# Performance work log

Hardware: AMD Instinct MI355X
Metric: run time of the kernel (lower is better)

Reference implementation:

```python
import jax, jax.numpy as jnp
import numpy as np
jax.config.update("jax_enable_x64", True)

B, S, E, H, L = 2, 1024, 768, 8, 8
FF, V = 2048, 32000
NT, REAL = 1, 512  # n_thoughts_taken, real_token_count


def _ln(x, g, b, eps=1e-5):
    m = jnp.mean(x, axis=-1, keepdims=True)
    v = jnp.var(x, axis=-1, keepdims=True)
    return (x - m) / jnp.sqrt(v + eps) * g + b


def setup_inputs() -> dict:
    key = jax.random.key(0)
    ks = jax.random.split(key, 12)
    f32 = jnp.float32
    rn = lambda k, shp, s=0.02: jax.random.normal(k, shp, f32) * s
    return {
        "x": jax.random.normal(ks[0], (B, S, E), f32),
        "tpe": rn(ks[1], (NT + 1, E)),
        "Wqkv": rn(ks[2], (L, 3 * E, E)),
        "bqkv": jnp.zeros((L, 3 * E), f32),
        "W1": rn(ks[3], (L, FF, E)),
        "b1": jnp.zeros((L, FF), f32),
        "W2": rn(ks[4], (L, E, FF)),
        "b2": jnp.zeros((L, E), f32),
        "g1": jnp.ones((L, E), f32),
        "be1": jnp.zeros((L, E), f32),
        "g2": jnp.ones((L, E), f32),
        "be2": jnp.zeros((L, E), f32),
        "gf": jnp.ones((E,), f32),
        "bf": jnp.zeros((E,), f32),
        "Wp1": rn(ks[5], (FF, E)),
        "bp1": jnp.zeros((FF,), f32),
        "Wp2": rn(ks[6], (V, FF)),
        "bp2": jnp.zeros((V,), f32),
        "Wv1": rn(ks[7], (FF, E)),
        "bv1": jnp.zeros((FF,), f32),
        "Wv2": rn(ks[8], (1, FF)),
        "bv2": jnp.zeros((1,), f32),
        "n_thoughts_taken": NT,
        "real_token_count": REAL,
    }


def reference(x, tpe, Wqkv, bqkv, W1, b1, W2, b2, g1, be1, g2, be2, gf, bf,
              Wp1, bp1, Wp2, bp2, Wv1, bv1, Wv2, bv2,
              n_thoughts_taken, real_token_count):
    Bs, Sq, Em = x.shape
    bs = int(n_thoughts_taken) + 1          # per-thought block size
    real = int(real_token_count)
    dh = Em // H

    # ---- DualPositionalEncoding (dropout=0) ----
    pos = np.arange(real)[:, None]
    div = np.exp(np.arange(0, Em, 2) * (-np.log(10000.0) / Em))
    pe = np.zeros((real, Em), np.float32)
    pe[:, 0::2] = np.sin(pos * div)
    pe[:, 1::2] = np.cos(pos * div)
    xb = x[:, :real * bs].reshape(Bs, real, bs, Em)
    xb = xb + jnp.asarray(pe)[None, :, None, :] + tpe[None, None, :bs, :]
    h = xb.reshape(Bs, real * bs, Em)
    pad = Sq - real * bs
    if pad > 0:
        h = jnp.pad(h, ((0, 0), (0, pad), (0, 0)))

    # ---- block-causal mask. NOTE: the original adds the BOOL mask to the
    # fp64 scores, so masked positions get +1.0 (not -inf). Faithful. ----
    i = np.arange(Sq)
    tok = i // bs
    p = i % bs
    M = ((tok[:, None] == tok[None, :]) & (p[None, :] >= p[:, None])) | \
        ((p[:, None] == 0) & (i[None, :] > i[:, None]) & (i[None, :] < real * bs))
    bias = jnp.asarray((M.T == 0).astype(np.float64))  # [S, S]
    scale = 1.0 / np.sqrt(dh)

    def layer(hc, params):
        Wq, bq, w1, b1_, w2, b2_, g1_, be1_, g2_, be2_ = params
        h64 = hc.astype(jnp.float64)
        qkv = h64 @ Wq.astype(jnp.float64).T + bq.astype(jnp.float64)
        q, k, v = jnp.split(qkv, 3, axis=-1)
        heads = lambda t: t.reshape(Bs, Sq, H, dh).transpose(0, 2, 1, 3)
        q, k, v = heads(q), heads(k), heads(v)
        scores = jnp.einsum('bhqd,bhkd->bhqk', q, k) * scale + bias
        w = jax.nn.softmax(scores, axis=-1)
        o = jnp.einsum('bhqk,bhkd->bhqd', w, v)
        o = o.transpose(0, 2, 1, 3).reshape(Bs, Sq, Em).astype(hc.dtype)
        # NOTE: original skips the attention out_proj entirely. Faithful.
        hc = _ln(hc + o, g1_, be1_)
        ff = jax.nn.gelu(hc @ w1.T + b1_, approximate=False) @ w2.T + b2_
        hc = _ln(hc + ff, g2_, be2_)
        return jnp.nan_to_num(hc), None

    h, _ = jax.lax.scan(layer, h, (Wqkv, bqkv, W1, b1, W2, b2, g1, be1, g2, be2))
    h = _ln(h, gf, bf)  # TransformerEncoder final norm

    act_idx = jnp.arange(real) * bs + n_thoughts_taken
    a = h[:, act_idx]  # [B, real, E]
    policy = jax.nn.gelu(a @ Wp1.T + bp1, approximate=False) @ Wp2.T + bp2
    value = jax.nn.gelu(a @ Wv1.T + bv1, approximate=False) @ Wv2.T + bv2
    return policy, value
```

## Files before the change

kernel.cpp:

```cpp
#include <hip/hip_runtime.h>
#include <math.h>

#define BB    2
#define SS    1024
#define EE    768
#define NH    8
#define DHD   96
#define NL    8
#define FFD   2048
#define VD    32000
#define REALC 512
#define MTOK  (BB*SS)
#define MACTN (BB*REALC)
#define QKVW  (3*EE)

#define QB 64
#define KB 64
#define KS_LD 104
#define VT_LD 72
#define P_LD  72

typedef __attribute__((ext_vector_type(8))) short bf16x8;
typedef __attribute__((ext_vector_type(4))) float f32x4;

static __device__ __forceinline__ float gelu_exact(float x) {
    return 0.5f * x * (1.0f + erff(x * 0.7071067811865476f));
}
static __device__ __forceinline__ unsigned short f2bf(float f) {
    unsigned int u = __builtin_bit_cast(unsigned int, f);
    unsigned int r = u + 0x7FFFu + ((u >> 16) & 1u);
    return (unsigned short)(r >> 16);
}
static __device__ __forceinline__ float bf2f(unsigned short u) {
    union { unsigned int i; float f; } v; v.i = ((unsigned int)u) << 16; return v.f;
}

#define GLDS16(gp, lp) __builtin_amdgcn_global_load_lds( \
    (const __attribute__((address_space(1))) void*)(gp), \
    (__attribute__((address_space(3))) void*)(lp), 16, 0, 0)

#define CN0 (NL*QKVW*EE)
#define CN1 (NL*FFD*EE)
#define CN2 (NL*EE*FFD)
#define CN3 (FFD*EE)
#define CN4 (FFD*EE)
#define CN5 (VD*FFD)
#define CB0 (CN0/4)
#define CB1 (CB0 + CN1/4)
#define CB2 (CB1 + CN2/4)
#define CB3 (CB2 + CN3/4)
#define CB4 (CB3 + CN4/4)
#define CB5 (CB4 + CN5/4)

__global__ __launch_bounds__(256) void convall_kernel(
    const float* __restrict__ s0, const float* __restrict__ s1,
    const float* __restrict__ s2, const float* __restrict__ s3,
    const float* __restrict__ s4, const float* __restrict__ s5,
    unsigned short* __restrict__ dst) {
    int i = blockIdx.x * 256 + threadIdx.x;
    const float* src;
    int loc;
    if      (i < CB0) { src = s0; loc = i; }
    else if (i < CB1) { src = s1; loc = i - CB0; }
    else if (i < CB2) { src = s2; loc = i - CB1; }
    else if (i < CB3) { src = s3; loc = i - CB2; }
    else if (i < CB4) { src = s4; loc = i - CB3; }
    else              { src = s5; loc = i - CB4; }
    float4 v = ((const float4*)src)[loc];
    ushort4 o;
    o.x = f2bf(v.x); o.y = f2bf(v.y); o.z = f2bf(v.z); o.w = f2bf(v.w);
    ((ushort4*)dst)[i] = o;
}

__global__ __launch_bounds__(256) void embed_kernel(const float* __restrict__ x,
                                                    const float* __restrict__ tpe,
                                                    float* __restrict__ h,
                                                    unsigned short* __restrict__ hb) {
    int idx = blockIdx.x * 256 + threadIdx.x;
    if (idx >= MTOK * EE) return;
    int e = idx % EE;
    int tok = idx / EE;
    int s = tok & (SS - 1);
    int r = s >> 1;
    int p = s & 1;
    int k2 = (e >> 1) * 2;
    float div = expf((float)k2 * (-9.210340371976184f / (float)EE));
    float ang = (float)r * div;
    float pe = (e & 1) ? cosf(ang) : sinf(ang);
    float v = x[idx] + pe + tpe[p * EE + e];
    h[idx] = v;
    hb[idx] = f2bf(v);
}

template<int MODE>
__global__ __launch_bounds__(256) void gemm64_kernel(
    const unsigned short* __restrict__ A, const unsigned short* __restrict__ W,
    const float* __restrict__ bias, float* __restrict__ Cf,
    unsigned short* __restrict__ Cb, unsigned short* __restrict__ CvT,
    int M, int N, int K, int ldc) {
    __shared__ unsigned short As[2][64 * 32];
    __shared__ unsigned short Bs[2][128 * 32];
    const int bm = blockIdx.y * 64;
    const int bn = blockIdx.x * 128;
    const int t = threadIdx.x;
    const int w = t >> 6;
    const int lane = t & 63;
    const int wm = (w >> 1) * 32;
    const int wn = (w & 1) * 64;
    f32x4 acc[2][4] = {};

    const int sr   = t >> 2;
    const int skey = (t >> 3) & 3;
    const int scol = ((t & 3) ^ skey) * 8;
    const unsigned short* gA = A + (size_t)(bm + sr) * K + scol;
    const unsigned short* gB = W + (size_t)(bn + sr) * K + scol;

    const int lc  = lane & 15;
    const int lr4 = lane >> 4;
    const int sl  = (lr4 ^ ((lc >> 1) & 3)) * 8;

    const int nsteps = K >> 5;
    GLDS16(gA,                  &As[0][w * 512]);
    GLDS16(gB,                  &Bs[0][w * 512]);
    GLDS16(gB + (size_t)64 * K, &Bs[0][2048 + w * 512]);
    __syncthreads();
    for (int kt = 0; kt < nsteps; ++kt) {
        const int cur = kt & 1;
        if (kt + 1 < nsteps) {
            const int k0 = (kt + 1) << 5;
            GLDS16(gA + k0,                  &As[cur ^ 1][w * 512]);
            GLDS16(gB + k0,                  &Bs[cur ^ 1][w * 512]);
            GLDS16(gB + (size_t)64 * K + k0, &Bs[cur ^ 1][2048 + w * 512]);
        }
        bf16x8 a[2], b[4];
#pragma unroll
        for (int mi = 0; mi < 2; ++mi)
            a[mi] = *(const bf16x8*)&As[cur][(wm + mi * 16 + lc) * 32 + sl];
#pragma unroll
        for (int ni = 0; ni < 4; ++ni)
            b[ni] = *(const bf16x8*)&Bs[cur][(wn + ni * 16 + lc) * 32 + sl];
#pragma unroll
        for (int mi = 0; mi < 2; ++mi)
#pragma unroll
            for (int ni = 0; ni < 4; ++ni)
                acc[mi][ni] = __builtin_amdgcn_mfma_f32_16x16x32_bf16(
                    a[mi], b[ni], acc[mi][ni], 0, 0, 0);
        __syncthreads();
    }

    const bool vpart = (MODE == 1) && (bn >= 2 * EE);
#pragma unroll
    for (int mi = 0; mi < 2; ++mi) {
#pragma unroll
        for (int ni = 0; ni < 4; ++ni) {
            const int c = bn + wn + ni * 16 + lc;
            const float bv = bias[c];
            const int rwb = bm + wm + mi * 16 + lr4 * 4;
            if (vpart) {
                ushort4 pk;
                pk.x = f2bf(acc[mi][ni][0] + bv);
                pk.y = f2bf(acc[mi][ni][1] + bv);
                pk.z = f2bf(acc[mi][ni][2] + bv);
                pk.w = f2bf(acc[mi][ni][3] + bv);
                *(ushort4*)&CvT[(size_t)(c - 2 * EE) * MTOK + rwb] = pk;
            } else {
#pragma unroll
                for (int r = 0; r < 4; ++r) {
                    float v = acc[mi][ni][r] + bv;
                    if (MODE == 3) {
                        v = gelu_exact(v);
                        Cb[(size_t)(rwb + r) * ldc + c] = f2bf(v);
                    } else if (MODE == 1) {
                        Cb[(size_t)(rwb + r) * ldc + c] = f2bf(v);
                    } else {
                        Cf[(size_t)(rwb + r) * ldc + c] = v;
                    }
                }
            }
        }
    }
}

__global__ __launch_bounds__(256, 2) void gemm_policy_kernel(
    const unsigned short* __restrict__ A, const unsigned short* __restrict__ W,
    const float* __restrict__ bias, float* __restrict__ C, int lda) {
    const int id = blockIdx.x;
    const int xcd = id & 7;
    const int rest = id >> 3;
    const int mt = rest & 7;
    const int ntile = (rest >> 3) * 8 + xcd;
    if (ntile >= VD / 256) return;
    const int bm = mt * 128;
    const int bn = ntile * 256;
    const int K = FFD;

    __shared__ unsigned short As[128 * 64];
    __shared__ unsigned short Bs[256 * 64];
    const int t = threadIdx.x;
    const int w = t >> 6;
    const int lane = t & 63;
    const int wm = (w >> 1) * 64;
    const int wn = (w & 1) * 128;
    f32x4 acc[4][8] = {};

    const int rr8  = (w << 3) + (lane >> 3);
    const int scol = (((lane & 7) ^ ((lane >> 3) & 7))) * 8;
    const unsigned short* gA = A + (size_t)(bm + rr8) * lda + scol;
    const unsigned short* gB = W + (size_t)(bn + rr8) * K + scol;

    const int lc  = lane & 15;
    const int lr4 = lane >> 4;
    const int key8 = lc & 7;

    for (int k0 = 0; k0 < K; k0 += 64) {
        __syncthreads();
#pragma unroll
        for (int i = 0; i < 4; ++i)
            GLDS16(gA + (size_t)(i * 32) * lda + k0, &As[((w << 3) + i * 32) * 64]);
#pragma unroll
        for (int i = 0; i < 8; ++i)
            GLDS16(gB + (size_t)(i * 32) * K + k0, &Bs[((w << 3) + i * 32) * 64]);
        __syncthreads();
#pragma unroll
        for (int ks = 0; ks < 2; ++ks) {
            const int sl = ((ks * 4 + lr4) ^ key8) * 8;
            bf16x8 a[4], b[8];
#pragma unroll
            for (int mi = 0; mi < 4; ++mi)
                a[mi] = *(const bf16x8*)&As[(wm + mi * 16 + lc) * 64 + sl];
#pragma unroll
            for (int ni = 0; ni < 8; ++ni)
                b[ni] = *(const bf16x8*)&Bs[(wn + ni * 16 + lc) * 64 + sl];
#pragma unroll
            for (int mi = 0; mi < 4; ++mi)
#pragma unroll
                for (int ni = 0; ni < 8; ++ni)
                    acc[mi][ni] = __builtin_amdgcn_mfma_f32_16x16x32_bf16(
                        a[mi], b[ni], acc[mi][ni], 0, 0, 0);
        }
    }
#pragma unroll
    for (int mi = 0; mi < 4; ++mi) {
#pragma unroll
        for (int ni = 0; ni < 8; ++ni) {
            const int c = bn + wn + ni * 16 + lc;
            const float bv = bias[c];
            const int rwb = bm + wm + mi * 16 + lr4 * 4;
#pragma unroll
            for (int r = 0; r < 4; ++r)
                C[(size_t)(rwb + r) * VD + c] = acc[mi][ni][r] + bv;
        }
    }
}

__global__ __launch_bounds__(256) void attn_mfma_kernel(
    const unsigned short* __restrict__ qkvb,
    const unsigned short* __restrict__ vT,
    float* __restrict__ o) {
    __shared__ unsigned short Ks[2][KB * KS_LD];
    __shared__ unsigned short VTs[2][DHD * VT_LD];
    __shared__ unsigned short Ps[QB * P_LD];

    const int bq = blockIdx.x * QB;
    const int hh = blockIdx.y & 7;
    const int b  = blockIdx.y >> 3;
    const int t = threadIdx.x;
    const int w = t >> 6;
    const int lane = t & 63;
    const int lr = lane >> 4;
    const int lc = lane & 15;
    const float scale = 0.10206207261596577f;

    const unsigned short* gK[3];
    const unsigned short* gV[3];
    int kwr[3], vwr[3];
#pragma unroll
    for (int it = 0; it < 3; ++it) {
        int flat = it * 256 + t;
        int kr = flat / 12;
        int d8 = (flat % 12) * 8;
        int d  = flat >> 3;
        int k8 = (flat & 7) * 8;
        gK[it] = qkvb + (size_t)(b * SS + kr) * QKVW + EE + hh * DHD + d8;
        gV[it] = vT + (size_t)(hh * DHD + d) * MTOK + b * SS + k8;
        kwr[it] = kr * KS_LD + d8;
        vwr[it] = d * VT_LD + k8;
    }

    bf16x8 qa[3];
    {
        const unsigned short* qrow = qkvb + (size_t)(b * SS + bq + w * 16 + lc) * QKVW + hh * DHD;
#pragma unroll
        for (int ks = 0; ks < 3; ++ks)
            qa[ks] = *(const bf16x8*)(qrow + ks * 32 + lr * 8);
    }

    f32x4 acc_o[6] = {};
    float m_st[4], l_st[4];
#pragma unroll
    for (int r = 0; r < 4; ++r) { m_st[r] = -1e30f; l_st[r] = 0.f; }
    const int q_row = lr << 2;
    const int qbase = bq + w * 16 + q_row;

    bf16x8 kst[3], vst[3];
#pragma unroll
    for (int it = 0; it < 3; ++it) {
        kst[it] = *(const bf16x8*)gK[it];
        vst[it] = *(const bf16x8*)gV[it];
    }
#pragma unroll
    for (int it = 0; it < 3; ++it) {
        *(bf16x8*)&Ks[0][kwr[it]] = kst[it];
        *(bf16x8*)&VTs[0][vwr[it]] = vst[it];
    }
    __syncthreads();

    const int NTILE = SS / KB;
    for (int kt = 0; kt < NTILE; ++kt) {
        const int cur = kt & 1;
        if (kt + 1 < NTILE) {
#pragma unroll
            for (int it = 0; it < 3; ++it) {
                kst[it] = *(const bf16x8*)(gK[it] + (size_t)(kt + 1) * KB * QKVW);
                vst[it] = *(const bf16x8*)(gV[it] + (kt + 1) * KB);
            }
        }

        f32x4 sfr[4] = {};
#pragma unroll
        for (int nf = 0; nf < 4; ++nf) {
#pragma unroll
            for (int ks = 0; ks < 3; ++ks) {
                bf16x8 kb = *(const bf16x8*)&Ks[cur][(nf * 16 + lc) * KS_LD + ks * 32 + lr * 8];
                sfr[nf] = __builtin_amdgcn_mfma_f32_16x16x32_bf16(qa[ks], kb, sfr[nf], 0, 0, 0);
            }
        }
        const int kbase = kt * KB;
#pragma unroll
        for (int nf = 0; nf < 4; ++nf) {
            const int k = kbase + nf * 16 + lc;
            const bool kodd = (k & 1);
#pragma unroll
            for (int r = 0; r < 4; ++r) {
                const int q = qbase + r;
                bool allowed = kodd ? (q == k) : (q >= k);
                sfr[nf][r] = sfr[nf][r] * scale + (allowed ? 0.f : 1.f);
            }
        }
        float corr[4];
#pragma unroll
        for (int r = 0; r < 4; ++r) {
            float v = fmaxf(fmaxf(sfr[0][r], sfr[1][r]), fmaxf(sfr[2][r], sfr[3][r]));
            v = fmaxf(v, __shfl_xor(v, 1)); v = fmaxf(v, __shfl_xor(v, 2));
            v = fmaxf(v, __shfl_xor(v, 4)); v = fmaxf(v, __shfl_xor(v, 8));
            float mn = fmaxf(m_st[r], v);
            corr[r] = __expf(m_st[r] - mn);
            m_st[r] = mn;
        }
        float rsum[4] = {0.f, 0.f, 0.f, 0.f};
#pragma unroll
        for (int nf = 0; nf < 4; ++nf) {
#pragma unroll
            for (int r = 0; r < 4; ++r) {
                float p = __expf(sfr[nf][r] - m_st[r]);
                rsum[r] += p;
                Ps[(w * 16 + q_row + r) * P_LD + nf * 16 + lc] = f2bf(p);
            }
        }
#pragma unroll
        for (int r = 0; r < 4; ++r) {
            float v = rsum[r];
            v += __shfl_xor(v, 1); v += __shfl_xor(v, 2);
            v += __shfl_xor(v, 4); v += __shfl_xor(v, 8);
            l_st[r] = l_st[r] * corr[r] + v;
        }
#pragma unroll
        for (int nf = 0; nf < 6; ++nf)
#pragma unroll
            for (int r = 0; r < 4; ++r)
                acc_o[nf][r] *= corr[r];
#pragma unroll
        for (int ks2 = 0; ks2 < 2; ++ks2) {
            bf16x8 pa = *(const bf16x8*)&Ps[(w * 16 + lc) * P_LD + ks2 * 32 + lr * 8];
#pragma unroll
            for (int nf = 0; nf < 6; ++nf) {
                bf16x8 vb = *(const bf16x8*)&VTs[cur][(nf * 16 + lc) * VT_LD + ks2 * 32 + lr * 8];
                acc_o[nf] = __builtin_amdgcn_mfma_f32_16x16x32_bf16(pa, vb, acc_o[nf], 0, 0, 0);
            }
        }

        if (kt + 1 < NTILE) {
#pragma unroll
            for (int it = 0; it < 3; ++it) {
                *(bf16x8*)&Ks[cur ^ 1][kwr[it]] = kst[it];
                *(bf16x8*)&VTs[cur ^ 1][vwr[it]] = vst[it];
            }
        }
        __syncthreads();
    }
#pragma unroll
    for (int nf = 0; nf < 6; ++nf) {
#pragma unroll
        for (int r = 0; r < 4; ++r) {
            const int q = bq + w * 16 + q_row + r;
            o[(size_t)(b * SS + q) * EE + hh * DHD + nf * 16 + lc] = acc_o[nf][r] / l_st[r];
        }
    }
}

template<bool GATHER>
__global__ __launch_bounds__(256) void ln_kernel(const float* __restrict__ a,
                                                 const float* __restrict__ res,
                                                 const float* __restrict__ g,
                                                 const float* __restrict__ beta,
                                                 float* __restrict__ outf,
                                                 unsigned short* __restrict__ outb) {
    __shared__ float rs[4], rs2[4];
    const int row = blockIdx.x;
    const int t = threadIdx.x;
    int src = row;
    if (GATHER) src = (row >> 9) * SS + ((row & 511) << 1) + 1;
    const float* pa = a + (size_t)src * EE;
    const float* pr = res ? res + (size_t)src * EE : nullptr;
    float x[3];
    float s = 0.f, s2 = 0.f;
#pragma unroll
    for (int i = 0; i < 3; ++i) {
        int e = t + i * 256;
        float v = pa[e] + (pr ? pr[e] : 0.f);
        x[i] = v; s += v; s2 += v * v;
    }
#pragma unroll
    for (int m = 1; m < 64; m <<= 1) {
        s  += __shfl_xor(s, m);
        s2 += __shfl_xor(s2, m);
    }
    if ((t & 63) == 0) { rs[t >> 6] = s; rs2[t >> 6] = s2; }
    __syncthreads();
    const float S  = rs[0] + rs[1] + rs[2] + rs[3];
    const float S2 = rs2[0] + rs2[1] + rs2[2] + rs2[3];
    const float mean = S * (1.0f / EE);
    const float var  = S2 * (1.0f / EE) - mean * mean;
    const float rstd = 1.0f / sqrtf(var + 1e-5f);
#pragma unroll
    for (int i = 0; i < 3; ++i) {
        int e = t + i * 256;
        float v = (x[i] - mean) * rstd * g[e] + beta[e];
        if (isnan(v)) v = 0.f;
        if (outf) outf[(size_t)row * EE + e] = v;
        if (outb) outb[(size_t)row * EE + e] = f2bf(v);
    }
}

__global__ __launch_bounds__(256) void value2_kernel(const unsigned short* __restrict__ v1,
                                                     const float* __restrict__ Wv2,
                                                     const float* __restrict__ bv2,
                                                     float* __restrict__ out, int ld) {
    __shared__ float red[4];
    const int row = blockIdx.x;
    const int t = threadIdx.x;
    const unsigned short* pr = v1 + (size_t)row * ld;
    float s = 0.f;
    for (int i = t; i < FFD; i += 256) s = fmaf(bf2f(pr[i]), Wv2[i], s);
#pragma unroll
    for (int m = 1; m < 64; m <<= 1) s += __shfl_xor(s, m);
    if ((t & 63) == 0) red[t >> 6] = s;
    __syncthreads();
    if (t == 0) out[row] = red[0] + red[1] + red[2] + red[3] + bv2[0];
}

extern "C" void kernel_launch(void* const* d_in, const int* in_sizes, int n_in,
                              void* d_out, int out_size, void* d_ws, size_t ws_size,
                              hipStream_t stream) {
    const float* x    = (const float*)d_in[0];
    const float* tpe  = (const float*)d_in[1];
    const float* Wqkv = (const float*)d_in[2];
    const float* bqkv = (const float*)d_in[3];
    const float* W1   = (const float*)d_in[4];
    const float* b1   = (const float*)d_in[5];
    const float* W2   = (const float*)d_in[6];
    const float* b2   = (const float*)d_in[7];
    const float* g1   = (const float*)d_in[8];
    const float* be1  = (const float*)d_in[9];
    const float* g2   = (const float*)d_in[10];
    const float* be2  = (const float*)d_in[11];
    const float* gf   = (const float*)d_in[12];
    const float* bf   = (const float*)d_in[13];
    const float* Wp1  = (const float*)d_in[14];
    const float* bp1  = (const float*)d_in[15];
    const float* Wp2  = (const float*)d_in[16];
    const float* bp2  = (const float*)d_in[17];
    const float* Wv1  = (const float*)d_in[18];
    const float* bv1  = (const float*)d_in[19];
    const float* Wv2  = (const float*)d_in[20];
    const float* bv2  = (const float*)d_in[21];

    float* ws  = (float*)d_ws;
    float* h   = ws;
    float* o   = h  + (size_t)MTOK * EE;
    float* hc  = o  + (size_t)MTOK * EE;
    float* ff2 = hc + (size_t)MTOK * EE;
    float* bias_cat = ff2 + (size_t)MTOK * EE;
    unsigned short* bws = (unsigned short*)(bias_cat + 4096);
    unsigned short* h_bf    = bws;
    unsigned short* hc_bf   = h_bf    + (size_t)MTOK * EE;
    unsigned short* ff1_bf  = hc_bf   + (size_t)MTOK * EE;
    unsigned short* act_bf  = ff1_bf  + (size_t)MTOK * FFD;
    unsigned short* p1v1_bf = act_bf  + (size_t)MACTN * EE;
    unsigned short* qkv_bf  = p1v1_bf + (size_t)MACTN * 2 * FFD;
    unsigned short* vT      = qkv_bf  + (size_t)MTOK * QKVW;
    unsigned short* wq_all  = vT      + (size_t)EE * MTOK;
    unsigned short* w1_all  = wq_all  + (size_t)CN0;
    unsigned short* w2_all  = w1_all  + (size_t)CN1;
    unsigned short* wp1_bf  = w2_all  + (size_t)CN2;
    unsigned short* wv1_bf  = wp1_bf  + (size_t)CN3;
    unsigned short* wp2_bf  = wv1_bf  + (size_t)CN4;
    (void)wv1_bf;

    float* pol = (float*)d_out;
    float* val = (float*)d_out + (size_t)MACTN * VD;

    const int C256 = 256;
#define NBLK(n) (((n) + 255) / 256)

    embed_kernel<<<NBLK(MTOK * EE), C256, 0, stream>>>(x, tpe, h, h_bf);

    convall_kernel<<<CB5 / 256, C256, 0, stream>>>(Wqkv, W1, W2, Wp1, Wv1, Wp2, wq_all);

    hipMemcpyAsync(bias_cat,        bp1, FFD * sizeof(float), hipMemcpyDeviceToDevice, stream);
    hipMemcpyAsync(bias_cat + FFD,  bv1, FFD * sizeof(float), hipMemcpyDeviceToDevice, stream);

    for (int l = 0; l < NL; ++l) {
        gemm64_kernel<1><<<dim3(QKVW / 128, MTOK / 64), C256, 0, stream>>>(
            h_bf, wq_all + (size_t)l * QKVW * EE, bqkv + (size_t)l * QKVW,
            nullptr, qkv_bf, vT, MTOK, QKVW, EE, QKVW);
        attn_mfma_kernel<<<dim3(SS / QB, BB * NH), C256, 0, stream>>>(qkv_bf, vT, o);
        ln_kernel<false><<<MTOK, C256, 0, stream>>>(h, o, g1 + l * EE, be1 + l * EE, hc, hc_bf);
        gemm64_kernel<3><<<dim3(FFD / 128, MTOK / 64), C256, 0, stream>>>(
            hc_bf, w1_all + (size_t)l * FFD * EE, b1 + (size_t)l * FFD,
            nullptr, ff1_bf, nullptr, MTOK, FFD, EE, FFD);
        gemm64_kernel<0><<<dim3(EE / 128, MTOK / 64), C256, 0, stream>>>(
            ff1_bf, w2_all + (size_t)l * EE * FFD, b2 + (size_t)l * EE,
            ff2, nullptr, nullptr, MTOK, EE, FFD, EE);
        ln_kernel<false><<<MTOK, C256, 0, stream>>>(hc, ff2, g2 + l * EE, be2 + l * EE, h, h_bf);
    }

    ln_kernel<true><<<MACTN, C256, 0, stream>>>(h, nullptr, gf, bf, nullptr, act_bf);

    gemm64_kernel<3><<<dim3(2 * FFD / 128, MACTN / 64), C256, 0, stream>>>(
        act_bf, wp1_bf, bias_cat, nullptr, p1v1_bf, nullptr, MACTN, 2 * FFD, EE, 2 * FFD);

    gemm_policy_kernel<<<1024, C256, 0, stream>>>(p1v1_bf, wp2_bf, bp2, pol, 2 * FFD);

    value2_kernel<<<MACTN, C256, 0, stream>>>(p1v1_bf + FFD, Wv2, bv2, val, 2 * FFD);
#undef NBLK
}
```

Baseline: 1.282 ms.

## Double-buffer policy GEMM with 8 waves and interleaved prefetch; fold bias copies into convert kernel

Rewrites the large vocabulary projection GEMM to use 512 threads (8 waves, each owning a 64x64 sub-tile) and double-buffered LDS. Next-tile global-to-LDS loads are split into three chunks that are interleaved with four MFMA quadrants, separated by barriers and s_setprio hints, so loads overlap with compute. This adds LDS usage and many more barriers per K step. It also drops two device-to-device hipMemcpyAsync calls for the concatenated bias by having extra blocks of the weight-conversion kernel copy it, which removes two small launches.

```diff
diff --git a/kernel.cpp b/kernel.cpp
--- a/kernel.cpp
+++ b/kernel.cpp
@@ -56,8 +56,18 @@
     const float* __restrict__ s0, const float* __restrict__ s1,
     const float* __restrict__ s2, const float* __restrict__ s3,
     const float* __restrict__ s4, const float* __restrict__ s5,
-    unsigned short* __restrict__ dst) {
+    unsigned short* __restrict__ dst,
+    const float* __restrict__ bp1, const float* __restrict__ bv1,
+    float* __restrict__ bias_cat) {
     int i = blockIdx.x * 256 + threadIdx.x;
+    if (i >= CB5) {
+        int j = i - CB5;
+        if (j < 1024) {
+            float4 v = (j < 512) ? ((const float4*)bp1)[j] : ((const float4*)bv1)[j - 512];
+            ((float4*)bias_cat)[j] = v;
+        }
+        return;
+    }
     const float* src;
     int loc;
     if      (i < CB0) { src = s0; loc = i; }
@@ -181,7 +191,7 @@
     }
 }
 
-__global__ __launch_bounds__(256, 2) void gemm_policy_kernel(
+__global__ __launch_bounds__(512, 2) void gemm_policy_kernel(
     const unsigned short* __restrict__ A, const unsigned short* __restrict__ W,
     const float* __restrict__ bias, float* __restrict__ C, int lda) {
     const int id = blockIdx.x;
@@ -194,55 +204,123 @@
     const int bn = ntile * 256;
     const int K = FFD;
 
-    __shared__ unsigned short As[128 * 64];
-    __shared__ unsigned short Bs[256 * 64];
+    __shared__ unsigned short As[2][128 * 64];
+    __shared__ unsigned short Bs[2][256 * 64];
     const int t = threadIdx.x;
     const int w = t >> 6;
     const int lane = t & 63;
-    const int wm = (w >> 1) * 64;
-    const int wn = (w & 1) * 128;
-    f32x4 acc[4][8] = {};
-
-    const int rr8  = (w << 3) + (lane >> 3);
-    const int scol = (((lane & 7) ^ ((lane >> 3) & 7))) * 8;
-    const unsigned short* gA = A + (size_t)(bm + rr8) * lda + scol;
-    const unsigned short* gB = W + (size_t)(bn + rr8) * K + scol;
+    const int wm = (w >> 2) * 64;
+    const int wn = (w & 3) * 64;
+    f32x4 acc[4][4] = {};
+
+    const int srow = t >> 3;
+    const int scol = ((t & 7) ^ (srow & 7)) * 8;
+    const unsigned short* gA = A + (size_t)(bm + srow) * lda + scol;
+    const unsigned short* gB = W + (size_t)(bn + srow) * K + scol;
+    const int lwb = (w * 8) * 64;
 
     const int lc  = lane & 15;
     const int lr4 = lane >> 4;
     const int key8 = lc & 7;
 
-    for (int k0 = 0; k0 < K; k0 += 64) {
+#define PSTG_A(buf, k0) do { \
+    GLDS16(gA + (k0),                    &As[buf][lwb]); \
+    GLDS16(gA + (size_t)64 * lda + (k0), &As[buf][64 * 64 + lwb]); } while (0)
+#define PSTG_B01(buf, k0) do { \
+    GLDS16(gB + (k0),                    &Bs[buf][lwb]); \
+    GLDS16(gB + (size_t)64 * K + (k0),   &Bs[buf][64 * 64 + lwb]); } while (0)
+#define PSTG_B23(buf, k0) do { \
+    GLDS16(gB + (size_t)128 * K + (k0),  &Bs[buf][128 * 64 + lwb]); \
+    GLDS16(gB + (size_t)192 * K + (k0),  &Bs[buf][192 * 64 + lwb]); } while (0)
+
+    PSTG_A(0, 0); PSTG_B01(0, 0); PSTG_B23(0, 0);
+    __syncthreads();
+
+    for (int kt = 0; kt < K / 64; ++kt) {
+        const int cur = kt & 1;
+        const unsigned short* Ac = As[cur];
+        const unsigned short* Bc = Bs[cur];
+        const int kn = (kt + 1) << 6;
+        const bool pf = (kt + 1 < K / 64);
+        bf16x8 a[4][2], b[4][2];
+#pragma unroll
+        for (int mi = 0; mi < 2; ++mi)
+#pragma unroll
+            for (int ks = 0; ks < 2; ++ks)
+                a[mi][ks] = *(const bf16x8*)&Ac[(wm + mi * 16 + lc) * 64 + ((ks * 4 + lr4) ^ key8) * 8];
+#pragma unroll
+        for (int ni = 0; ni < 2; ++ni)
+#pragma unroll
+            for (int ks = 0; ks < 2; ++ks)
+                b[ni][ks] = *(const bf16x8*)&Bc[(wn + ni * 16 + lc) * 64 + ((ks * 4 + lr4) ^ key8) * 8];
+        if (pf) PSTG_A(cur ^ 1, kn);
+        __builtin_amdgcn_s_barrier();
+        __builtin_amdgcn_s_setprio(1);
+#pragma unroll
+        for (int mi = 0; mi < 2; ++mi)
+#pragma unroll
+            for (int ni = 0; ni < 2; ++ni)
+#pragma unroll
+                for (int ks = 0; ks < 2; ++ks)
+                    acc[mi][ni] = __builtin_amdgcn_mfma_f32_16x16x32_bf16(
+                        a[mi][ks], b[ni][ks], acc[mi][ni], 0, 0, 0);
+        __builtin_amdgcn_s_setprio(0);
+        __builtin_amdgcn_s_barrier();
+#pragma unroll
+        for (int ni = 2; ni < 4; ++ni)
+#pragma unroll
+            for (int ks = 0; ks < 2; ++ks)
+                b[ni][ks] = *(const bf16x8*)&Bc[(wn + ni * 16 + lc) * 64 + ((ks * 4 + lr4) ^ key8) * 8];
+        if (pf) PSTG_B01(cur ^ 1, kn);
+        __builtin_amdgcn_s_barrier();
+        __builtin_amdgcn_s_setprio(1);
+#pragma unroll
+        for (int mi = 0; mi < 2; ++mi)
+#pragma unroll
+            for (int ni = 2; ni < 4; ++ni)
+#pragma unroll
+                for (int ks = 0; ks < 2; ++ks)
+                    acc[mi][ni] = __builtin_amdgcn_mfma_f32_16x16x32_bf16(
+                        a[mi][ks], b[ni][ks], acc[mi][ni], 0, 0, 0);
+        __builtin_amdgcn_s_setprio(0);
+        __builtin_amdgcn_s_barrier();
+#pragma unroll
+        for (int mi = 2; mi < 4; ++mi)
+#pragma unroll
+            for (int ks = 0; ks < 2; ++ks)
+                a[mi][ks] = *(const bf16x8*)&Ac[(wm + mi * 16 + lc) * 64 + ((ks * 4 + lr4) ^ key8) * 8];
+        if (pf) PSTG_B23(cur ^ 1, kn);
+        __builtin_amdgcn_s_barrier();
+        __builtin_amdgcn_s_setprio(1);
+#pragma unroll
+        for (int mi = 2; mi < 4; ++mi)
+#pragma unroll
+            for (int ni = 2; ni < 4; ++ni)
+#pragma unroll
+                for (int ks = 0; ks < 2; ++ks)
+                    acc[mi][ni] = __builtin_amdgcn_mfma_f32_16x16x32_bf16(
+                        a[mi][ks], b[ni][ks], acc[mi][ni], 0, 0, 0);
+        __builtin_amdgcn_s_setprio(0);
+        __builtin_amdgcn_s_barrier();
+        __builtin_amdgcn_s_setprio(1);
+#pragma unroll
+        for (int mi = 2; mi < 4; ++mi)
+#pragma unroll
+            for (int ni = 0; ni < 2; ++ni)
+#pragma unroll
+                for (int ks = 0; ks < 2; ++ks)
+                    acc[mi][ni] = __builtin_amdgcn_mfma_f32_16x16x32_bf16(
+                        a[mi][ks], b[ni][ks], acc[mi][ni], 0, 0, 0);
+        __builtin_amdgcn_s_setprio(0);
         __syncthreads();
-#pragma unroll
-        for (int i = 0; i < 4; ++i)
-            GLDS16(gA + (size_t)(i * 32) * lda + k0, &As[((w << 3) + i * 32) * 64]);
-#pragma unroll
-        for (int i = 0; i < 8; ++i)
-            GLDS16(gB + (size_t)(i * 32) * K + k0, &Bs[((w << 3) + i * 32) * 64]);
-        __syncthreads();
-#pragma unroll
-        for (int ks = 0; ks < 2; ++ks) {
-            const int sl = ((ks * 4 + lr4) ^ key8) * 8;
-            bf16x8 a[4], b[8];
-#pragma unroll
-            for (int mi = 0; mi < 4; ++mi)
-                a[mi] = *(const bf16x8*)&As[(wm + mi * 16 + lc) * 64 + sl];
-#pragma unroll
-            for (int ni = 0; ni < 8; ++ni)
-                b[ni] = *(const bf16x8*)&Bs[(wn + ni * 16 + lc) * 64 + sl];
-#pragma unroll
-            for (int mi = 0; mi < 4; ++mi)
-#pragma unroll
-                for (int ni = 0; ni < 8; ++ni)
-                    acc[mi][ni] = __builtin_amdgcn_mfma_f32_16x16x32_bf16(
-                        a[mi], b[ni], acc[mi][ni], 0, 0, 0);
-        }
-    }
+    }
+#undef PSTG_A
+#undef PSTG_B01
+#undef PSTG_B23
 #pragma unroll
     for (int mi = 0; mi < 4; ++mi) {
 #pragma unroll
-        for (int ni = 0; ni < 8; ++ni) {
+        for (int ni = 0; ni < 4; ++ni) {
             const int c = bn + wn + ni * 16 + lc;
             const float bv = bias[c];
             const int rwb = bm + wm + mi * 16 + lr4 * 4;
@@ -525,10 +603,8 @@
 
     embed_kernel<<<NBLK(MTOK * EE), C256, 0, stream>>>(x, tpe, h, h_bf);
 
-    convall_kernel<<<CB5 / 256, C256, 0, stream>>>(Wqkv, W1, W2, Wp1, Wv1, Wp2, wq_all);
-
-    hipMemcpyAsync(bias_cat,        bp1, FFD * sizeof(float), hipMemcpyDeviceToDevice, stream);
-    hipMemcpyAsync(bias_cat + FFD,  bv1, FFD * sizeof(float), hipMemcpyDeviceToDevice, stream);
+    convall_kernel<<<CB5 / 256 + 4, C256, 0, stream>>>(
+        Wqkv, W1, W2, Wp1, Wv1, Wp2, wq_all, bp1, bv1, bias_cat);
 
     for (int l = 0; l < NL; ++l) {
         gemm64_kernel<1><<<dim3(QKVW / 128, MTOK / 64), C256, 0, stream>>>(
@@ -550,7 +626,7 @@
     gemm64_kernel<3><<<dim3(2 * FFD / 128, MACTN / 64), C256, 0, stream>>>(
         act_bf, wp1_bf, bias_cat, nullptr, p1v1_bf, nullptr, MACTN, 2 * FFD, EE, 2 * FFD);
 
-    gemm_policy_kernel<<<1024, C256, 0, stream>>>(p1v1_bf, wp2_bf, bp2, pol, 2 * FFD);
+    gemm_policy_kernel<<<1024, 512, 0, stream>>>(p1v1_bf, wp2_bf, bp2, pol, 2 * FFD);
 
     value2_kernel<<<MACTN, C256, 0, stream>>>(p1v1_bf + FFD, Wv2, bv2, val, 2 * FFD);
 #undef NBLK
```

New measurement: 1.356 ms. 5.8% more time.
